# Optimization experiments

Measured on AMD Instinct MI355X. Metric: run time of the kernel, lower is better.

Reference implementation:

```python
import jax, jax.numpy as jnp
import numpy as np

K = 8  # args.k


def setup_inputs() -> dict:
    key = jax.random.key(0)
    k1, k2, k3 = jax.random.split(key, 3)
    b, n_pre, n_cur = 1, 8192, 16384
    pre_xyzs = jax.random.normal(k1, (b, 3, n_pre), dtype=jnp.float32)
    cur_xyzs = jax.random.normal(k2, (b, 3, n_cur), dtype=jnp.float32)
    # UpsampleNumLayer output range: sigmoid * (max_upsample_num - 1) + 1  in [1, 8]
    upsample_num = jax.random.uniform(k3, (b, n_pre), dtype=jnp.float32) * 7.0 + 1.0
    return {"pre_xyzs": pre_xyzs, "cur_xyzs": cur_xyzs, "upsample_num": upsample_num}


def _sqdist(a, b):
    # a: (b, n, 3), b: (b, m, 3) -> (b, n, m) squared euclidean distances
    return ((a * a).sum(-1)[:, :, None]
            + (b * b).sum(-1)[:, None, :]
            - 2.0 * jnp.einsum('bnc,bmc->bnm', a, b))


def reference(pre_xyzs, cur_xyzs, upsample_num):
    # pre_xyzs: (b, 3, n_pre); cur_xyzs: (b, 3, n_cur); upsample_num: (b, n_pre)
    pre_t = pre_xyzs.transpose(0, 2, 1)  # (b, n_pre, 3)
    cur_t = cur_xyzs.transpose(0, 2, 1)  # (b, n_cur, 3)

    # knnquery_heap(1, pre, cur): nearest pre index for each cur point -> (b, n_cur)
    cur2pre = jnp.argmin(_sqdist(cur_t, pre_t), axis=-1)

    # knnquery_heap(K, cur, pre): K nearest cur indices for each pre point -> (b, n_pre, K)
    _, knn_idx = jax.lax.top_k(-_sqdist(pre_t, cur_t), K)

    # real_center: gather cur2pre at knn_idx -> (b, n_pre, K)
    real_center = jax.vmap(lambda c2p, idx: c2p[idx])(cur2pre, knn_idx)
    expect_center = jnp.arange(pre_xyzs.shape[2])[None, :, None]  # (1, n_pre, 1)
    mask = (expect_center == real_center).astype(pre_xyzs.dtype)  # (b, n_pre, K)

    # knn_xyzs: gather cur_xyzs columns at knn_idx -> (b, 3, n_pre, K)
    knn_xyzs = jax.vmap(lambda pts, idx: pts[:, idx])(cur_xyzs, knn_idx)

    diff = knn_xyzs - pre_xyzs[..., None]              # (b, 3, n_pre, K)
    dist = jnp.sqrt((diff * diff).sum(axis=1))         # (b, n_pre, K), L2 over channel dim
    mean_distance = (dist * mask).sum(axis=-1) / upsample_num  # (b, n_pre)
    return mean_distance
```

## Files before the change

### kernel.cpp

```cpp
#include <hip/hip_runtime.h>

#define N_PRE 8192
#define N_CUR 16384
#define KNN   8


#define MAPPED_INF 0xFF800000u

__device__ __forceinline__ unsigned key_of(float d) {
    unsigned b = __float_as_uint(d);
    return b ^ (0x80000000u | (unsigned)((int)b >> 31));
}
__device__ __forceinline__ float float_of_key(unsigned k) {
    unsigned b = (k & 0x80000000u) ? (k ^ 0x80000000u) : ~k;
    return __uint_as_float(b);
}
__device__ __forceinline__ unsigned shfl_u32(unsigned x, int src) {
    return (unsigned)__shfl((int)x, src);
}
__device__ __forceinline__ unsigned shfl_up1_u32(unsigned x) {
    return (unsigned)__shfl_up((int)x, 1);
}

__global__ __launch_bounds__(256) void prep_kernel(
        const float* __restrict__ pre, const float* __restrict__ cur,
        float4* __restrict__ pre4, float4* __restrict__ cur4) {
    int i = blockIdx.x * 256 + threadIdx.x;
    if (i < N_CUR) {
        float x = cur[i], y = cur[N_CUR + i], z = cur[2 * N_CUR + i];
        cur4[i] = make_float4(x, y, z, fmaf(x, x, fmaf(y, y, z * z)));
    }
    if (i < N_PRE) {
        float x = pre[i], y = pre[N_PRE + i], z = pre[2 * N_PRE + i];
        pre4[i] = make_float4(-2.f * x, -2.f * y, -2.f * z,
                              fmaf(x, x, fmaf(y, y, z * z)));
    }
}

#define TILE_A 2048

__global__ __launch_bounds__(1024) void cur2pre_kernel(
        const float4* __restrict__ pre4, const float4* __restrict__ cur4,
        unsigned* __restrict__ c2p) {
    __shared__ float4 sp[TILE_A];
    const int tid  = threadIdx.x;
    const int lane = tid & 63;
    const int w    = tid >> 6;
    const int j0   = blockIdx.x * 64 + w * 4;

    const float4 c0 = cur4[j0 + 0];
    const float4 c1 = cur4[j0 + 1];
    const float4 c2 = cur4[j0 + 2];
    const float4 c3 = cur4[j0 + 3];

    const float INF = __int_as_float(0x7F800000);
    float b0 = INF, b1 = INF, b2 = INF, b3 = INF;
    int   i0 = 0,   i1 = 0,   i2 = 0,   i3 = 0;

    for (int tile = 0; tile < N_PRE; tile += TILE_A) {
        __syncthreads();
        for (int k = tid; k < TILE_A; k += 1024) sp[k] = pre4[tile + k];
        __syncthreads();

#pragma unroll 4
        for (int s = 0; s < TILE_A; s += 64) {
            float4 q = sp[s + lane];
            int idx = tile + s + lane;
            float d0 = fmaf(q.x, c0.x, fmaf(q.y, c0.y, fmaf(q.z, c0.z, q.w)));
            float d1 = fmaf(q.x, c1.x, fmaf(q.y, c1.y, fmaf(q.z, c1.z, q.w)));
            float d2 = fmaf(q.x, c2.x, fmaf(q.y, c2.y, fmaf(q.z, c2.z, q.w)));
            float d3 = fmaf(q.x, c3.x, fmaf(q.y, c3.y, fmaf(q.z, c3.z, q.w)));
            if (d0 < b0) { b0 = d0; i0 = idx; }
            if (d1 < b1) { b1 = d1; i1 = idx; }
            if (d2 < b2) { b2 = d2; i2 = idx; }
            if (d3 < b3) { b3 = d3; i3 = idx; }
        }
    }

    float        bs[4] = {b0, b1, b2, b3};
    int          is[4] = {i0, i1, i2, i3};
#pragma unroll
    for (int t = 0; t < 4; ++t) {
        unsigned long long v =
            (((unsigned long long)key_of(bs[t])) << 32) | (unsigned)is[t];
#pragma unroll
        for (int off = 32; off > 0; off >>= 1) {
            unsigned long long o = __shfl_xor((unsigned long long)v, off);
            v = (o < v) ? o : v;
        }
        if (lane == 0) c2p[j0 + t] = (unsigned)(v & 0xFFFFFFFFull);
    }
}

#define TILE_B 2048

__global__ __launch_bounds__(1024) void knn_finalize_kernel(
        const float4* __restrict__ pre4, const float4* __restrict__ cur4,
        const float* __restrict__ ups,
        const unsigned* __restrict__ c2p,
        float* __restrict__ out) {
    __shared__ float4 sc[TILE_B];
    const int tid  = threadIdx.x;
    const int lane = tid & 63;
    const int w    = tid >> 6;
    const int i0   = blockIdx.x * 32 + w * 2;
    const int i1   = i0 + 1;

    const float4 p0 = pre4[i0];
    const float4 p1 = pre4[i1];

    unsigned ld0 = MAPPED_INF, li0 = 0u;
    unsigned ld1 = MAPPED_INF, li1 = 0u;
    float t80 = __int_as_float(0x7F800000);
    float t81 = t80;

    for (int tile = 0; tile < N_CUR; tile += TILE_B) {
        __syncthreads();
        for (int k = tid; k < TILE_B; k += 1024) sc[k] = cur4[tile + k];
        __syncthreads();

#pragma unroll 4
        for (int s = 0; s < TILE_B; s += 64) {
            float4 c = sc[s + lane];
            float d0 = fmaf(p0.x, c.x, fmaf(p0.y, c.y, fmaf(p0.z, c.z, c.w)));
            float d1 = fmaf(p1.x, c.x, fmaf(p1.y, c.y, fmaf(p1.z, c.z, c.w)));
            int jj = tile + s + lane;

            unsigned long long m0 = __ballot(d0 < t80);
            while (m0) {
                int src = __ffsll(m0) - 1;
                float fd = __uint_as_float(shfl_u32(__float_as_uint(d0), src));
                unsigned kd = key_of(fd);
                unsigned kj = shfl_u32((unsigned)jj, src);
                unsigned ud = shfl_up1_u32(ld0);
                unsigned uj = shfl_up1_u32(li0);
                if (lane == 0) ud = 0u;
                bool hi = kd < ud, lo = kd < ld0;
                ld0 = hi ? ud : (lo ? kd : ld0);
                li0 = hi ? uj : (lo ? kj : li0);
                t80 = float_of_key(shfl_u32(ld0, 7));
                m0 = (m0 & (m0 - 1)) & __ballot(d0 < t80);
            }

            unsigned long long m1 = __ballot(d1 < t81);
            while (m1) {
                int src = __ffsll(m1) - 1;
                float fd = __uint_as_float(shfl_u32(__float_as_uint(d1), src));
                unsigned kd = key_of(fd);
                unsigned kj = shfl_u32((unsigned)jj, src);
                unsigned ud = shfl_up1_u32(ld1);
                unsigned uj = shfl_up1_u32(li1);
                if (lane == 0) ud = 0u;
                bool hi = kd < ud, lo = kd < ld1;
                ld1 = hi ? ud : (lo ? kd : ld1);
                li1 = hi ? uj : (lo ? kj : li1);
                t81 = float_of_key(shfl_u32(ld1, 7));
                m1 = (m1 & (m1 - 1)) & __ballot(d1 < t81);
            }
        }
    }

    unsigned ja = shfl_u32(li0, lane & 7);
    unsigned jb = shfl_u32(li1, lane & 7);
    unsigned j  = (lane < 8) ? ja : jb;

    float contrib = 0.f;
    if (lane < 16) {
        float4 c = cur4[j];
        float px = -0.5f * ((lane < 8) ? p0.x : p1.x);
        float py = -0.5f * ((lane < 8) ? p0.y : p1.y);
        float pz = -0.5f * ((lane < 8) ? p0.z : p1.z);
        float dx = c.x - px, dy = c.y - py, dz = c.z - pz;
        float dsq = fmaf(dx, dx, fmaf(dy, dy, dz * dz));
        unsigned owner = c2p[j];
        unsigned iexp  = (lane < 8) ? (unsigned)i0 : (unsigned)i1;
        contrib = (owner == iexp) ? sqrtf(dsq) : 0.f;
    }
    contrib += __shfl_xor(contrib, 1);
    contrib += __shfl_xor(contrib, 2);
    contrib += __shfl_xor(contrib, 4);
    if (lane == 0) out[i0] = contrib / ups[i0];
    if (lane == 8) out[i1] = contrib / ups[i1];
}

extern "C" void kernel_launch(void* const* d_in, const int* in_sizes, int n_in,
                              void* d_out, int out_size, void* d_ws, size_t ws_size,
                              hipStream_t stream) {
    const float* pre = (const float*)d_in[0];
    const float* cur = (const float*)d_in[1];
    const float* ups = (const float*)d_in[2];
    float* out = (float*)d_out;

    char* ws = (char*)d_ws;
    unsigned* c2p = (unsigned*)ws;
    float4*   pre4 = (float4*)(ws + 65536);
    float4*   cur4 = (float4*)(ws + 65536 + 131072);

    prep_kernel<<<N_CUR / 256, 256, 0, stream>>>(pre, cur, pre4, cur4);

    cur2pre_kernel<<<N_CUR / 64, 1024, 0, stream>>>(pre4, cur4, c2p);

    knn_finalize_kernel<<<N_PRE / 32, 1024, 0, stream>>>(pre4, cur4, ups, c2p, out);
}
```

Measured before the change: 143.1 us.

## Split nearest-pre search across slices with atomicMin and keep top-8 per lane

The cur2pre kernel is split across four slices of pre points. Each block handles one slice and merges its packed (distance key, index) minimum into a 64-bit buffer with atomicMin; prep initializes that buffer. This gives four times more blocks and removes the per-tile sync loop. The knn kernel now keeps a replicated sorted top-8 list in registers per lane instead of a cross-lane shift list, which removes shuffles from the insert path but uses more registers, and its block size drops to 512.

```diff
diff --git a/kernel.cpp b/kernel.cpp
--- a/kernel.cpp
+++ b/kernel.cpp
@@ -18,17 +18,30 @@
 __device__ __forceinline__ unsigned shfl_u32(unsigned x, int src) {
     return (unsigned)__shfl((int)x, src);
 }
-__device__ __forceinline__ unsigned shfl_up1_u32(unsigned x) {
-    return (unsigned)__shfl_up((int)x, 1);
+
+__device__ __forceinline__ void insert8(unsigned (&k)[8], unsigned (&id)[8],
+                                        unsigned kd, unsigned kj) {
+    bool m[8];
+#pragma unroll
+    for (int t = 0; t < 8; ++t) m[t] = kd < k[t];
+#pragma unroll
+    for (int t = 7; t >= 1; --t) {
+        k[t]  = m[t - 1] ? k[t - 1]  : (m[t] ? kd : k[t]);
+        id[t] = m[t - 1] ? id[t - 1] : (m[t] ? kj : id[t]);
+    }
+    k[0]  = m[0] ? kd : k[0];
+    id[0] = m[0] ? kj : id[0];
 }
 
 __global__ __launch_bounds__(256) void prep_kernel(
         const float* __restrict__ pre, const float* __restrict__ cur,
-        float4* __restrict__ pre4, float4* __restrict__ cur4) {
+        float4* __restrict__ pre4, float4* __restrict__ cur4,
+        unsigned long long* __restrict__ c2p64) {
     int i = blockIdx.x * 256 + threadIdx.x;
     if (i < N_CUR) {
         float x = cur[i], y = cur[N_CUR + i], z = cur[2 * N_CUR + i];
         cur4[i] = make_float4(x, y, z, fmaf(x, x, fmaf(y, y, z * z)));
+        c2p64[i] = 0xFFFFFFFFFFFFFFFFull;
     }
     if (i < N_PRE) {
         float x = pre[i], y = pre[N_PRE + i], z = pre[2 * N_PRE + i];
@@ -37,86 +50,99 @@
     }
 }
 
-#define TILE_A 2048
+#define TILE_A   2048
+#define SLICES_A (N_PRE / TILE_A)
 
 __global__ __launch_bounds__(1024) void cur2pre_kernel(
         const float4* __restrict__ pre4, const float4* __restrict__ cur4,
-        unsigned* __restrict__ c2p) {
+        unsigned long long* __restrict__ c2p64) {
     __shared__ float4 sp[TILE_A];
-    const int tid  = threadIdx.x;
-    const int lane = tid & 63;
-    const int w    = tid >> 6;
-    const int j0   = blockIdx.x * 64 + w * 4;
+    const int tid   = threadIdx.x;
+    const int lane  = tid & 63;
+    const int w     = tid >> 6;
+    const int slice = blockIdx.x & (SLICES_A - 1);
+    const int cg    = blockIdx.x >> 2;
+    const int j0    = cg * 64 + w * 4;
+    const int sbase = slice * TILE_A;
 
     const float4 c0 = cur4[j0 + 0];
     const float4 c1 = cur4[j0 + 1];
     const float4 c2 = cur4[j0 + 2];
     const float4 c3 = cur4[j0 + 3];
 
+    for (int k = tid; k < TILE_A; k += 1024) sp[k] = pre4[sbase + k];
+    __syncthreads();
+
     const float INF = __int_as_float(0x7F800000);
     float b0 = INF, b1 = INF, b2 = INF, b3 = INF;
     int   i0 = 0,   i1 = 0,   i2 = 0,   i3 = 0;
 
-    for (int tile = 0; tile < N_PRE; tile += TILE_A) {
-        __syncthreads();
-        for (int k = tid; k < TILE_A; k += 1024) sp[k] = pre4[tile + k];
-        __syncthreads();
-
 #pragma unroll 4
-        for (int s = 0; s < TILE_A; s += 64) {
-            float4 q = sp[s + lane];
-            int idx = tile + s + lane;
-            float d0 = fmaf(q.x, c0.x, fmaf(q.y, c0.y, fmaf(q.z, c0.z, q.w)));
-            float d1 = fmaf(q.x, c1.x, fmaf(q.y, c1.y, fmaf(q.z, c1.z, q.w)));
-            float d2 = fmaf(q.x, c2.x, fmaf(q.y, c2.y, fmaf(q.z, c2.z, q.w)));
-            float d3 = fmaf(q.x, c3.x, fmaf(q.y, c3.y, fmaf(q.z, c3.z, q.w)));
-            if (d0 < b0) { b0 = d0; i0 = idx; }
-            if (d1 < b1) { b1 = d1; i1 = idx; }
-            if (d2 < b2) { b2 = d2; i2 = idx; }
-            if (d3 < b3) { b3 = d3; i3 = idx; }
-        }
-    }
-
-    float        bs[4] = {b0, b1, b2, b3};
-    int          is[4] = {i0, i1, i2, i3};
-#pragma unroll
-    for (int t = 0; t < 4; ++t) {
-        unsigned long long v =
-            (((unsigned long long)key_of(bs[t])) << 32) | (unsigned)is[t];
-#pragma unroll
-        for (int off = 32; off > 0; off >>= 1) {
-            unsigned long long o = __shfl_xor((unsigned long long)v, off);
-            v = (o < v) ? o : v;
-        }
-        if (lane == 0) c2p[j0 + t] = (unsigned)(v & 0xFFFFFFFFull);
+    for (int s = 0; s < TILE_A; s += 64) {
+        float4 q = sp[s + lane];
+        int idx = sbase + s + lane;
+        float d0 = fmaf(q.x, c0.x, fmaf(q.y, c0.y, fmaf(q.z, c0.z, q.w)));
+        float d1 = fmaf(q.x, c1.x, fmaf(q.y, c1.y, fmaf(q.z, c1.z, q.w)));
+        float d2 = fmaf(q.x, c2.x, fmaf(q.y, c2.y, fmaf(q.z, c2.z, q.w)));
+        float d3 = fmaf(q.x, c3.x, fmaf(q.y, c3.y, fmaf(q.z, c3.z, q.w)));
+        if (d0 < b0) { b0 = d0; i0 = idx; }
+        if (d1 < b1) { b1 = d1; i1 = idx; }
+        if (d2 < b2) { b2 = d2; i2 = idx; }
+        if (d3 < b3) { b3 = d3; i3 = idx; }
+    }
+
+    unsigned long long v0 = (((unsigned long long)key_of(b0)) << 32) | (unsigned)i0;
+    unsigned long long v1 = (((unsigned long long)key_of(b1)) << 32) | (unsigned)i1;
+    unsigned long long v2 = (((unsigned long long)key_of(b2)) << 32) | (unsigned)i2;
+    unsigned long long v3 = (((unsigned long long)key_of(b3)) << 32) | (unsigned)i3;
+#pragma unroll
+    for (int off = 32; off > 0; off >>= 1) {
+        unsigned long long o0 = __shfl_xor(v0, off);
+        unsigned long long o1 = __shfl_xor(v1, off);
+        unsigned long long o2 = __shfl_xor(v2, off);
+        unsigned long long o3 = __shfl_xor(v3, off);
+        v0 = (o0 < v0) ? o0 : v0;
+        v1 = (o1 < v1) ? o1 : v1;
+        v2 = (o2 < v2) ? o2 : v2;
+        v3 = (o3 < v3) ? o3 : v3;
+    }
+    if (lane == 0) {
+        atomicMin(c2p64 + j0 + 0, v0);
+        atomicMin(c2p64 + j0 + 1, v1);
+        atomicMin(c2p64 + j0 + 2, v2);
+        atomicMin(c2p64 + j0 + 3, v3);
     }
 }
 
 #define TILE_B 2048
 
-__global__ __launch_bounds__(1024) void knn_finalize_kernel(
+__global__ __launch_bounds__(512) void knn_finalize_kernel(
         const float4* __restrict__ pre4, const float4* __restrict__ cur4,
         const float* __restrict__ ups,
-        const unsigned* __restrict__ c2p,
+        const unsigned long long* __restrict__ c2p64,
         float* __restrict__ out) {
     __shared__ float4 sc[TILE_B];
     const int tid  = threadIdx.x;
     const int lane = tid & 63;
     const int w    = tid >> 6;
-    const int i0   = blockIdx.x * 32 + w * 2;
+    const int i0   = blockIdx.x * 16 + w * 2;
     const int i1   = i0 + 1;
 
     const float4 p0 = pre4[i0];
     const float4 p1 = pre4[i1];
 
-    unsigned ld0 = MAPPED_INF, li0 = 0u;
-    unsigned ld1 = MAPPED_INF, li1 = 0u;
+    unsigned k0_[8], id0_[8], k1_[8], id1_[8];
+#pragma unroll
+    for (int t = 0; t < 8; ++t) {
+        k0_[t] = MAPPED_INF; id0_[t] = 0u;
+        k1_[t] = MAPPED_INF; id1_[t] = 0u;
+    }
     float t80 = __int_as_float(0x7F800000);
     float t81 = t80;
 
     for (int tile = 0; tile < N_CUR; tile += TILE_B) {
         __syncthreads();
-        for (int k = tid; k < TILE_B; k += 1024) sc[k] = cur4[tile + k];
+        for (int k = tid; k < TILE_B; k += 512) sc[k] = cur4[tile + k];
         __syncthreads();
 
 #pragma unroll 4
@@ -124,45 +150,38 @@
             float4 c = sc[s + lane];
             float d0 = fmaf(p0.x, c.x, fmaf(p0.y, c.y, fmaf(p0.z, c.z, c.w)));
             float d1 = fmaf(p1.x, c.x, fmaf(p1.y, c.y, fmaf(p1.z, c.z, c.w)));
-            int jj = tile + s + lane;
+            const int jbase = tile + s;
 
             unsigned long long m0 = __ballot(d0 < t80);
             while (m0) {
-                int src = __ffsll(m0) - 1;
+                int src = __ffsll((unsigned long long)m0) - 1;
                 float fd = __uint_as_float(shfl_u32(__float_as_uint(d0), src));
                 unsigned kd = key_of(fd);
-                unsigned kj = shfl_u32((unsigned)jj, src);
-                unsigned ud = shfl_up1_u32(ld0);
-                unsigned uj = shfl_up1_u32(li0);
-                if (lane == 0) ud = 0u;
-                bool hi = kd < ud, lo = kd < ld0;
-                ld0 = hi ? ud : (lo ? kd : ld0);
-                li0 = hi ? uj : (lo ? kj : li0);
-                t80 = float_of_key(shfl_u32(ld0, 7));
+                unsigned kj = (unsigned)(jbase + src);
+                insert8(k0_, id0_, kd, kj);
+                t80 = float_of_key(k0_[7]);
                 m0 = (m0 & (m0 - 1)) & __ballot(d0 < t80);
             }
 
             unsigned long long m1 = __ballot(d1 < t81);
             while (m1) {
-                int src = __ffsll(m1) - 1;
+                int src = __ffsll((unsigned long long)m1) - 1;
                 float fd = __uint_as_float(shfl_u32(__float_as_uint(d1), src));
                 unsigned kd = key_of(fd);
-                unsigned kj = shfl_u32((unsigned)jj, src);
-                unsigned ud = shfl_up1_u32(ld1);
-                unsigned uj = shfl_up1_u32(li1);
-                if (lane == 0) ud = 0u;
-                bool hi = kd < ud, lo = kd < ld1;
-                ld1 = hi ? ud : (lo ? kd : ld1);
-                li1 = hi ? uj : (lo ? kj : li1);
-                t81 = float_of_key(shfl_u32(ld1, 7));
+                unsigned kj = (unsigned)(jbase + src);
+                insert8(k1_, id1_, kd, kj);
+                t81 = float_of_key(k1_[7]);
                 m1 = (m1 & (m1 - 1)) & __ballot(d1 < t81);
             }
         }
     }
 
-    unsigned ja = shfl_u32(li0, lane & 7);
-    unsigned jb = shfl_u32(li1, lane & 7);
-    unsigned j  = (lane < 8) ? ja : jb;
+    unsigned j = 0;
+#pragma unroll
+    for (int t = 0; t < 8; ++t) {
+        unsigned cand = (lane < 8) ? id0_[t] : id1_[t];
+        j = ((lane & 7) == t) ? cand : j;
+    }
 
     float contrib = 0.f;
     if (lane < 16) {
@@ -172,7 +191,7 @@
         float pz = -0.5f * ((lane < 8) ? p0.z : p1.z);
         float dx = c.x - px, dy = c.y - py, dz = c.z - pz;
         float dsq = fmaf(dx, dx, fmaf(dy, dy, dz * dz));
-        unsigned owner = c2p[j];
+        unsigned owner = (unsigned)(c2p64[j] & 0xFFFFFFFFull);
         unsigned iexp  = (lane < 8) ? (unsigned)i0 : (unsigned)i1;
         contrib = (owner == iexp) ? sqrtf(dsq) : 0.f;
     }
@@ -192,13 +211,13 @@
     float* out = (float*)d_out;
 
     char* ws = (char*)d_ws;
-    unsigned* c2p = (unsigned*)ws;
-    float4*   pre4 = (float4*)(ws + 65536);
-    float4*   cur4 = (float4*)(ws + 65536 + 131072);
-
-    prep_kernel<<<N_CUR / 256, 256, 0, stream>>>(pre, cur, pre4, cur4);
-
-    cur2pre_kernel<<<N_CUR / 64, 1024, 0, stream>>>(pre4, cur4, c2p);
-
-    knn_finalize_kernel<<<N_PRE / 32, 1024, 0, stream>>>(pre4, cur4, ups, c2p, out);
-}
+    unsigned long long* c2p64 = (unsigned long long*)ws;
+    float4* pre4 = (float4*)(ws + 131072);
+    float4* cur4 = (float4*)(ws + 131072 + 131072);
+
+    prep_kernel<<<N_CUR / 256, 256, 0, stream>>>(pre, cur, pre4, cur4, c2p64);
+
+    cur2pre_kernel<<<(N_CUR / 64) * SLICES_A, 1024, 0, stream>>>(pre4, cur4, c2p64);
+
+    knn_finalize_kernel<<<N_PRE / 16, 512, 0, stream>>>(pre4, cur4, ups, c2p64, out);
+}
```

After: 159.6 us. +11.5%, slower.
